# Kernel tuning notes

Measured on AMD Instinct MI355X. Metric: run time of the kernel, lower is better.

Reference implementation:

```python
import jax, jax.numpy as jnp
import numpy as np

B, N, S, C1, C2 = 8, 8192, 2048, 128, 256
IN_CH = C1 + C2
MLP = [256, 128]
EPS_INTERP = 1e-8
EPS_BN = 1e-5


def setup_inputs() -> dict:
    key = jax.random.key(0)
    ks = jax.random.split(key, 8)
    inp = {
        "xyz1": jax.random.normal(ks[0], (B, 3, N), dtype=jnp.float32),
        "xyz2": jax.random.normal(ks[1], (B, 3, S), dtype=jnp.float32),
        "points1": jax.random.normal(ks[2], (B, C1, N), dtype=jnp.float32),
        "points2": jax.random.normal(ks[3], (B, C2, S), dtype=jnp.float32),
        # Conv1d(k=1) weights as [out, in] matrices, plus BN gamma/beta
        "W1": jax.random.normal(ks[4], (MLP[0], IN_CH), dtype=jnp.float32) * 0.02,
        "b1": jnp.zeros((MLP[0],), dtype=jnp.float32),
        "g1": jnp.ones((MLP[0],), dtype=jnp.float32),
        "be1": jnp.zeros((MLP[0],), dtype=jnp.float32),
        "W2": jax.random.normal(ks[5], (MLP[1], MLP[0]), dtype=jnp.float32) * 0.02,
        "b2": jnp.zeros((MLP[1],), dtype=jnp.float32),
        "g2": jnp.ones((MLP[1],), dtype=jnp.float32),
        "be2": jnp.zeros((MLP[1],), dtype=jnp.float32),
    }
    return inp


def _conv_bn_relu(x, W, b, g, be):
    # x: [B, N, Cin]; 1x1 Conv1d == per-point matmul; BN over (batch, length) per channel (training-mode stats)
    y = jnp.einsum('bnc,oc->bno', x, W) + b
    m = jnp.mean(y, axis=(0, 1))
    v = jnp.var(y, axis=(0, 1))
    return jax.nn.relu((y - m) * jax.lax.rsqrt(v + EPS_BN) * g + be)


def reference(xyz1, xyz2, points1, points2, W1, b1, g1, be1, W2, b2, g2, be2):
    x1 = xyz1.transpose(0, 2, 1)   # [B, N, 3]
    x2 = xyz2.transpose(0, 2, 1)   # [B, S, 3]
    p2 = points2.transpose(0, 2, 1)  # [B, S, C2]
    p1 = points1.transpose(0, 2, 1)  # [B, N, C1]

    # squared pairwise distances [B, N, S]
    d = (jnp.sum(x1 * x1, axis=-1, keepdims=True)
         - 2.0 * jnp.einsum('bnd,bsd->bns', x1, x2)
         + jnp.sum(x2 * x2, axis=-1)[:, None, :])

    # 3 nearest neighbors (smallest distances)
    neg_d, idx = jax.lax.top_k(-d, 3)          # idx: [B, N, 3]
    d3 = -neg_d                                 # [B, N, 3]
    recip = 1.0 / (d3 + EPS_INTERP)
    w = recip / jnp.sum(recip, axis=-1, keepdims=True)  # [B, N, 3]

    gathered = jax.vmap(lambda p, i: p[i])(p2, idx)     # [B, N, 3, C2]
    interp = jnp.sum(gathered * w[..., None], axis=2)   # [B, N, C2]

    x = jnp.concatenate([p1, interp], axis=-1)          # [B, N, C1+C2]
    x = _conv_bn_relu(x, W1, b1, g1, be1)
    x = _conv_bn_relu(x, W2, b2, g2, be2)
    return x.transpose(0, 2, 1)                         # [B, mlp[-1], N]
```

## Files before the change

kernel.cpp:

```cpp
#include <hip/hip_runtime.h>
#include <stdint.h>

#define B_ 8
#define N_ 8192
#define S_ 2048
#define C1_ 128
#define C2_ 256
#define IN_ 384
#define H1_ 256
#define H2_ 128
#define M_ (B_*N_)

typedef short bf16x8 __attribute__((ext_vector_type(8)));
typedef float f32x4 __attribute__((ext_vector_type(4)));

__device__ __forceinline__ float bf2f(unsigned short s){
  union { unsigned int u; float f; } x; x.u = ((unsigned int)s) << 16; return x.f;
}
__device__ __forceinline__ unsigned short f2bf(float f){
  union { float f; unsigned int u; } x; x.f = f;
  unsigned int u = x.u;
  unsigned int r = (u + 0x7FFFu + ((u >> 16) & 1u)) >> 16;
  return (unsigned short)r;
}

__device__ __forceinline__ size_t fragaddr(int m, int k, int K){
  return ((size_t)((m >> 4) * (K >> 5) + (k >> 5)) << 9)
       + (size_t)((((k >> 3) & 3) << 7) + ((m & 15) << 3) + (k & 7));
}

__device__ __forceinline__ void gload_lds16(const unsigned short* g, unsigned short* l){
  __builtin_amdgcn_global_load_lds(
      (const __attribute__((address_space(1))) unsigned int*)g,
      (__attribute__((address_space(3))) unsigned int*)l, 16, 0, 0);
}

__global__ __launch_bounds__(256) void prep_fused_kernel(const float* W1, const float* W2,
                                                         const float* p2, const float* p1,
                                                         const float* xyz2, float4* ptsg,
                                                         unsigned short* w1b, unsigned short* w2b,
                                                         float* stats, unsigned short* p2t,
                                                         unsigned short* x){
  __shared__ float tile[32][33];
  int bx = blockIdx.x;
  if (bx < 384){
    int i = bx * 256 + threadIdx.x;
    if (i < 256*384){
      int row = i / 384, col = i - row*384;
      w1b[fragaddr(row, col, 384)] = f2bf(W1[i]);
    }
    if (i < 128*256){
      int row = i >> 8, col = i & 255;
      w2b[fragaddr(row, col, 256)] = f2bf(W2[i]);
    }
    if (i < 1536) stats[i] = 0.f;
    return;
  }
  if (bx < 448){
    int i = (bx - 384) * 256 + threadIdx.x;
    int b = i >> 11, s = i & 2047;
    const float* src = xyz2 + (size_t)b * 3 * S_;
    float px = src[s], py = src[S_ + s], pz = src[2*S_ + s];
    ptsg[i] = make_float4(-2.f*px, -2.f*py, -2.f*pz, px*px + py*py + pz*pz);
    return;
  }
  int tx = threadIdx.x & 31, ty = threadIdx.x >> 5;
  if (bx < 4544){
    int id = bx - 448;
    int b = id >> 9, rem = id & 511;
    int l0 = (rem & 63) * 32, r0 = (rem >> 6) * 32;
    const float* src = p2 + (size_t)b * C2_ * S_;
    #pragma unroll
    for (int rr = ty; rr < 32; rr += 8)
      tile[rr][tx] = src[(size_t)(r0 + rr) * S_ + l0 + tx];
    __syncthreads();
    unsigned short* dst = p2t + (size_t)b * S_ * C2_;
    #pragma unroll
    for (int rr = ty; rr < 32; rr += 8)
      dst[(size_t)(l0 + rr) * C2_ + r0 + tx] = f2bf(tile[tx][rr]);
    return;
  }
  {
    int id = bx - 4544;
    int b = id >> 10, rem = id & 1023;
    int l0 = (rem & 255) * 32, r0 = (rem >> 8) * 32;
    const float* src = p1 + (size_t)b * C1_ * N_;
    #pragma unroll
    for (int rr = ty; rr < 32; rr += 8)
      tile[rr][tx] = src[(size_t)(r0 + rr) * N_ + l0 + tx];
    __syncthreads();
    #pragma unroll
    for (int rr = ty; rr < 32; rr += 8){
      int g = b * N_ + l0 + rr;
      size_t a = ((size_t)((g >> 4)*12 + (r0 >> 5)) << 9)
               + (size_t)((((tx >> 3) & 3) << 7) + ((g & 15) << 3) + (tx & 7));
      x[a] = f2bf(tile[tx][rr]);
    }
  }
}

#define PIECES_ 8
#define SPP_ (S_ / PIECES_)

__device__ __forceinline__ void insert_k(float& k0, float& k1, float& k2, float x){
  k2 = __builtin_amdgcn_fmed3f(k1, k2, x);
  k1 = __builtin_amdgcn_fmed3f(k0, k1, x);
  k0 = fminf(k0, x);
}

__device__ __forceinline__ void insert3(float& d0, float& d1, float& d2,
                                        int& i0, int& i1, int& i2,
                                        float x, int s){
  bool b0 = x < d0, b1 = x < d1, b2 = x < d2;
  i2 = b1 ? i1 : (b2 ? s : i2);
  i1 = b0 ? i0 : (b1 ? s : i1);
  i0 = b0 ? s : i0;
  d2 = __builtin_amdgcn_fmed3f(d1, d2, x);
  d1 = __builtin_amdgcn_fmed3f(d0, d1, x);
  d0 = fminf(d0, x);
}

__global__ __launch_bounds__(256, 8) void knn_kernel(const float* __restrict__ xyz1,
                                                     const float4* __restrict__ ptsg,
                                                     float* __restrict__ partd,
                                                     int* __restrict__ parti){
  __shared__ float4 pts[SPP_];
  int b = blockIdx.y, piece = blockIdx.z;
  int n = blockIdx.x * 256 + threadIdx.x;
  int base = piece * SPP_;
  const float4* __restrict__ cp = ptsg + (size_t)b * S_ + base;
  pts[threadIdx.x] = cp[threadIdx.x];

  const float* __restrict__ x1 = xyz1 + (size_t)b * 3 * N_;
  float ax = x1[n], ay = x1[N_ + n], az = x1[2*N_ + n];
  float x1sq = ax*ax + ay*ay + az*az;

  const float KINIT = __uint_as_float(0x7F000000u);
  float k[2][3];
  k[0][0]=k[0][1]=k[0][2]=KINIT;
  k[1][0]=k[1][1]=k[1][2]=KINIT;

  for (int s = 0; s < SPP_; s += 8){
    #pragma unroll
    for (int u = 0; u < 8; u++){
      float4 c = cp[s + u];
      float dd = fmaf(ax, c.x, fmaf(ay, c.y, fmaf(az, c.z, c.w + x1sq)));
      float key = __uint_as_float((__float_as_uint(dd) & 0xFFFFFF00u) | (unsigned)(s + u));
      int L = u & 1;
      insert_k(k[L][0], k[L][1], k[L][2], key);
    }
  }
  float e0 = k[0][0], e1 = k[0][1], e2 = k[0][2];
  insert_k(e0, e1, e2, k[1][0]);
  insert_k(e0, e1, e2, k[1][1]);
  insert_k(e0, e1, e2, k[1][2]);

  __syncthreads();
  float ed[3]; int ei[3];
  float ev[3] = {e0, e1, e2};
  #pragma unroll
  for (int j = 0; j < 3; j++){
    int li = (int)(__float_as_uint(ev[j]) & 0xFFu);
    float4 c = pts[li];
    float dd = fmaf(ax, c.x, fmaf(ay, c.y, fmaf(az, c.z, c.w + x1sq)));
    ed[j] = fmaxf(dd, 0.f);
    ei[j] = base + li;
  }

  size_t g = (size_t)b * N_ + n;
  partd[(piece*3 + 0)*(size_t)M_ + g] = ed[0];
  partd[(piece*3 + 1)*(size_t)M_ + g] = ed[1];
  partd[(piece*3 + 2)*(size_t)M_ + g] = ed[2];
  parti[(piece*3 + 0)*(size_t)M_ + g] = ei[0];
  parti[(piece*3 + 1)*(size_t)M_ + g] = ei[1];
  parti[(piece*3 + 2)*(size_t)M_ + g] = ei[2];
}

__global__ __launch_bounds__(256) void interp_kernel(const float* partd, const int* parti,
                                                     const unsigned short* p2t, unsigned short* x){
  __shared__ int   sidx[16][3];
  __shared__ float swgt[16][3];
  int t = threadIdx.x;
  int base = blockIdx.x * 16;
  if (t < 16){
    size_t g = (size_t)base + t;
    float d0 = partd[0*(size_t)M_ + g], d1 = partd[1*(size_t)M_ + g], d2 = partd[2*(size_t)M_ + g];
    int   i0 = parti[0*(size_t)M_ + g], i1 = parti[1*(size_t)M_ + g], i2 = parti[2*(size_t)M_ + g];
    #pragma unroll
    for (int p = 1; p < PIECES_; p++)
      #pragma unroll
      for (int j = 0; j < 3; j++)
        insert3(d0, d1, d2, i0, i1, i2,
                partd[(p*3 + j)*(size_t)M_ + g], parti[(p*3 + j)*(size_t)M_ + g]);
    float r0 = 1.f/(d0 + 1e-8f), r1 = 1.f/(d1 + 1e-8f), r2 = 1.f/(d2 + 1e-8f);
    float rs = 1.f/(r0 + r1 + r2);
    sidx[t][0] = i0; sidx[t][1] = i1; sidx[t][2] = i2;
    swgt[t][0] = r0*rs; swgt[t][1] = r1*rs; swgt[t][2] = r2*rs;
  }
  __syncthreads();
  size_t suboff = (size_t)((((t >> 3) & 3) << 7) + (t & 7));
  for (int k = 0; k < 16; k++){
    int g = base + k;
    int b = g >> 13;
    const unsigned short* p = p2t + (size_t)b * S_ * C2_;
    float v = swgt[k][0]*bf2f(p[(size_t)sidx[k][0]*C2_ + t])
            + swgt[k][1]*bf2f(p[(size_t)sidx[k][1]*C2_ + t])
            + swgt[k][2]*bf2f(p[(size_t)sidx[k][2]*C2_ + t]);
    size_t a = ((size_t)((g >> 4)*12 + 4 + (t >> 5)) << 9) + suboff + (size_t)((g & 15) << 3);
    x[a] = f2bf(v);
  }
}

__device__ __forceinline__ bf16x8 bn_relu_frag(bf16x8 v, const float* a, const float* c, int kb){
  union { bf16x8 h; unsigned short s[8]; } u; u.h = v;
  union { float4 v4; float f[4]; } a0, a1, c0, c1;
  a0.v4 = *(const float4*)(a + kb);  a1.v4 = *(const float4*)(a + kb + 4);
  c0.v4 = *(const float4*)(c + kb);  c1.v4 = *(const float4*)(c + kb + 4);
  #pragma unroll
  for (int j = 0; j < 4; j++){
    float f0 = fmaf(a0.f[j], bf2f(u.s[j]),     c0.f[j]);
    float f1 = fmaf(a1.f[j], bf2f(u.s[j + 4]), c1.f[j]);
    u.s[j]     = f2bf(fmaxf(f0, 0.f));
    u.s[j + 4] = f2bf(fmaxf(f1, 0.f));
  }
  return u.h;
}

template<int K, bool HAS_AFF, bool OUT_FRAG>
__global__ __launch_bounds__(256) void gemm_lds_kernel(
    const unsigned short* __restrict__ A, const unsigned short* __restrict__ Wf,
    unsigned short* __restrict__ Cout, int Ntot,
    float* sumv, float* sqv, const float* aff_a, const float* aff_c)
{
  constexpr int KT = K / 32;
  __shared__ unsigned short smA[128*64];
  __shared__ unsigned short smB[128*64];
  __shared__ float ldsStat[256];

  const int t = threadIdx.x;
  const int lane = t & 63, wave = t >> 6;
  const int ln = lane & 15, lq = lane >> 4;
  const int wm = wave >> 1, wn = wave & 1;
  const int mtb = blockIdx.x * 8;
  const int ntb = blockIdx.y * 8;
  const int mtw = mtb + wm * 4;
  const int n0  = blockIdx.y * 128 + wn * 64;

  ldsStat[t] = 0.f;

  const int c0 = 2*wave, c1 = 2*wave + 1;

  const f32x4 fzero = {0.f, 0.f, 0.f, 0.f};
  f32x4 acc[4][4];
  #pragma unroll
  for (int i = 0; i < 4; i++)
    #pragma unroll
    for (int j = 0; j < 4; j++) acc[i][j] = fzero;

  for (int kk = 0; kk < KT; kk += 2){
    #pragma unroll
    for (int q = 0; q < 2; q++){
      gload_lds16(A  + (((size_t)((mtb + c0)*KT + kk + q)) << 9) + lane*8,
                  &smA[((c0*2 + q) << 9) + lane*8]);
      gload_lds16(A  + (((size_t)((mtb + c1)*KT + kk + q)) << 9) + lane*8,
                  &smA[((c1*2 + q) << 9) + lane*8]);
      gload_lds16(Wf + (((size_t)((ntb + c0)*KT + kk + q)) << 9) + lane*8,
                  &smB[((c0*2 + q) << 9) + lane*8]);
      gload_lds16(Wf + (((size_t)((ntb + c1)*KT + kk + q)) << 9) + lane*8,
                  &smB[((c1*2 + q) << 9) + lane*8]);
    }
    __syncthreads();
    #pragma unroll
    for (int q = 0; q < 2; q++){
      bf16x8 af[4], bf[4];
      #pragma unroll
      for (int i = 0; i < 4; i++)
        af[i] = *(const bf16x8*)(&smA[(((wm*4 + i)*2 + q) << 9) + lane*8]);
      #pragma unroll
      for (int j = 0; j < 4; j++)
        bf[j] = *(const bf16x8*)(&smB[(((wn*4 + j)*2 + q) << 9) + lane*8]);
      if (HAS_AFF){
        const int kb = (kk + q)*32 + lq*8;
        #pragma unroll
        for (int i = 0; i < 4; i++) af[i] = bn_relu_frag(af[i], aff_a, aff_c, kb);
      }
      #pragma unroll
      for (int i = 0; i < 4; i++)
        #pragma unroll
        for (int j = 0; j < 4; j++)
          acc[i][j] = __builtin_amdgcn_mfma_f32_16x16x32_bf16(af[i], bf[j], acc[i][j], 0, 0, 0);
    }
    __syncthreads();
  }

  #pragma unroll
  for (int j = 0; j < 4; j++){
    int ncol = n0 + j*16 + ln;
    float s = 0.f, q = 0.f;
    #pragma unroll
    for (int i = 0; i < 4; i++){
      #pragma unroll
      for (int r = 0; r < 4; r++){
        float v = acc[i][j][r];
        if (OUT_FRAG){
          size_t a = ((size_t)((mtw + i)*8 + (ncol >> 5)) << 9)
                   + (size_t)((((ncol >> 3) & 3) << 7) + ((lq*4 + r) << 3) + (ncol & 7));
          Cout[a] = f2bf(v);
        } else {
          Cout[((size_t)((mtw + i)*16 + lq*4 + r)) * Ntot + ncol] = f2bf(v);
        }
        s += v; q += v*v;
      }
    }
    s += __shfl_xor(s, 16); s += __shfl_xor(s, 32);
    q += __shfl_xor(q, 16); q += __shfl_xor(q, 32);
    if (lq == 0){
      int colLocal = wn*64 + j*16 + ln;
      atomicAdd(&ldsStat[colLocal], s);
      atomicAdd(&ldsStat[128 + colLocal], q);
    }
  }
  __syncthreads();
  {
    float v = ldsStat[t];
    int col = blockIdx.y*128 + (t & 127);
    atomicAdd((t < 128 ? &sumv[col] : &sqv[col]), v);
  }
}

__global__ void finalize_kernel(const float* sum, const float* sq, const float* g, const float* be,
                                float* a_out, float* c_out, int C){
  int c = threadIdx.x;
  if (c < C){
    float mean = sum[c] * (1.f / M_);
    float var  = sq[c]  * (1.f / M_) - mean*mean;
    float a = g[c] * rsqrtf(var + 1e-5f);
    a_out[c] = a;
    c_out[c] = fmaf(-mean, a, be[c]);
  }
}

__global__ __launch_bounds__(256) void out_kernel(const unsigned short* y2, const float* a2,
                                                  const float* c2, float* out){
  __shared__ float lds[64][65];
  int t  = threadIdx.x;
  int b  = blockIdx.z;
  int n0 = blockIdx.y * 64;
  int c0 = blockIdx.x * 64;
  int cc = t & 63, tr = t >> 6;
  float a = a2[c0 + cc], cadd = c2[c0 + cc];
  #pragma unroll
  for (int ph = 0; ph < 16; ph++){
    int nr = tr + ph*4;
    unsigned short v = y2[((size_t)(b*N_ + n0 + nr)) * H2_ + c0 + cc];
    lds[nr][cc] = fmaxf(fmaf(a, bf2f(v), cadd), 0.f);
  }
  __syncthreads();
  #pragma unroll
  for (int ph = 0; ph < 16; ph++){
    int cr = tr + ph*4;
    out[((size_t)(b*H2_ + c0 + cr)) * N_ + n0 + cc] = lds[cc][cr];
  }
}

extern "C" void kernel_launch(void* const* d_in, const int* in_sizes, int n_in,
                              void* d_out, int out_size, void* d_ws, size_t ws_size,
                              hipStream_t stream){
  const float* xyz1 = (const float*)d_in[0];
  const float* xyz2 = (const float*)d_in[1];
  const float* p1   = (const float*)d_in[2];
  const float* p2   = (const float*)d_in[3];
  const float* W1   = (const float*)d_in[4];
  const float* g1   = (const float*)d_in[6];
  const float* be1  = (const float*)d_in[7];
  const float* W2   = (const float*)d_in[8];
  const float* g2   = (const float*)d_in[10];
  const float* be2  = (const float*)d_in[11];
  float* out = (float*)d_out;

  char* ws = (char*)d_ws;
  unsigned short* x    = (unsigned short*)(ws + 0);
  unsigned short* p2t  = (unsigned short*)(ws + 50331648);
  unsigned short* y1   = (unsigned short*)(ws + 58720256);
  unsigned short* y2   = (unsigned short*)(ws + 92274688);
  unsigned short* w1b  = (unsigned short*)(ws + 109051904);
  unsigned short* w2b  = (unsigned short*)(ws + 109248512);
  float*          stats= (float*)(ws + 110886912);
  float* sum1 = stats;        float* sq1 = stats + 256;
  float* sum2 = stats + 512;  float* sq2 = stats + 640;
  float* a1   = stats + 768;  float* c1  = stats + 1024;
  float* a2   = stats + 1280; float* c2  = stats + 1408;
  float* partd = (float*)y1;
  int*   parti = (int*)(y1 + 6291456);
  float4* ptsg = (float4*)y2;

  prep_fused_kernel<<<12736, 256, 0, stream>>>(W1, W2, p2, p1, xyz2, ptsg, w1b, w2b, stats, p2t, x);
  knn_kernel<<<dim3(32, 8, PIECES_), 256, 0, stream>>>(xyz1, ptsg, partd, parti);
  interp_kernel<<<4096, 256, 0, stream>>>(partd, parti, p2t, x);
  gemm_lds_kernel<384, false, true><<<dim3(512, 2), 256, 0, stream>>>(
      x, w1b, y1, 256, sum1, sq1, nullptr, nullptr);
  finalize_kernel<<<1, 256, 0, stream>>>(sum1, sq1, g1, be1, a1, c1, 256);
  gemm_lds_kernel<256, true, false><<<dim3(512, 1), 256, 0, stream>>>(
      y1, w2b, y2, 128, sum2, sq2, a1, c1);
  finalize_kernel<<<1, 256, 0, stream>>>(sum2, sq2, g2, be2, a2, c2, 128);
  out_kernel<<<dim3(2, 128, 8), 256, 0, stream>>>(y2, a2, c2, out);
}
```

Baseline: 265.7 us.

## Double-buffer LDS tiles in GEMM to overlap global loads with MFMA

Splits the A and B shared-memory tiles into two buffers and issues the global-to-LDS loads for the next K step before computing on the current one. This is meant to hide load latency behind the MFMA work and cut one barrier per iteration. In exchange LDS use doubles to about 64KB per block, which may lower occupancy, and the loop is now fully unrolled.

```diff
diff --git a/kernel.cpp b/kernel.cpp
--- a/kernel.cpp
+++ b/kernel.cpp
@@ -233,8 +233,9 @@
     float* sumv, float* sqv, const float* aff_a, const float* aff_c)
 {
   constexpr int KT = K / 32;
-  __shared__ unsigned short smA[128*64];
-  __shared__ unsigned short smB[128*64];
+  constexpr int NI = KT / 2;
+  __shared__ unsigned short smA[2][128*64];
+  __shared__ unsigned short smB[2][128*64];
   __shared__ float ldsStat[256];
 
   const int t = threadIdx.x;
@@ -250,6 +251,20 @@
 
   const int c0 = 2*wave, c1 = 2*wave + 1;
 
+  auto stage = [&](int buf, int kk){
+    #pragma unroll
+    for (int q = 0; q < 2; q++){
+      gload_lds16(A  + (((size_t)((mtb + c0)*KT + kk + q)) << 9) + lane*8,
+                  &smA[buf][((c0*2 + q) << 9) + lane*8]);
+      gload_lds16(A  + (((size_t)((mtb + c1)*KT + kk + q)) << 9) + lane*8,
+                  &smA[buf][((c1*2 + q) << 9) + lane*8]);
+      gload_lds16(Wf + (((size_t)((ntb + c0)*KT + kk + q)) << 9) + lane*8,
+                  &smB[buf][((c0*2 + q) << 9) + lane*8]);
+      gload_lds16(Wf + (((size_t)((ntb + c1)*KT + kk + q)) << 9) + lane*8,
+                  &smB[buf][((c1*2 + q) << 9) + lane*8]);
+    }
+  };
+
   const f32x4 fzero = {0.f, 0.f, 0.f, 0.f};
   f32x4 acc[4][4];
   #pragma unroll
@@ -257,28 +272,23 @@
     #pragma unroll
     for (int j = 0; j < 4; j++) acc[i][j] = fzero;
 
-  for (int kk = 0; kk < KT; kk += 2){
+  stage(0, 0);
+  __syncthreads();
+
+  #pragma unroll
+  for (int it = 0; it < NI; ++it){
+    const int cur = it & 1;
+    if (it + 1 < NI) stage(cur ^ 1, (it + 1)*2);
+    const int kk = it*2;
     #pragma unroll
     for (int q = 0; q < 2; q++){
-      gload_lds16(A  + (((size_t)((mtb + c0)*KT + kk + q)) << 9) + lane*8,
-                  &smA[((c0*2 + q) << 9) + lane*8]);
-      gload_lds16(A  + (((size_t)((mtb + c1)*KT + kk + q)) << 9) + lane*8,
-                  &smA[((c1*2 + q) << 9) + lane*8]);
-      gload_lds16(Wf + (((size_t)((ntb + c0)*KT + kk + q)) << 9) + lane*8,
-                  &smB[((c0*2 + q) << 9) + lane*8]);
-      gload_lds16(Wf + (((size_t)((ntb + c1)*KT + kk + q)) << 9) + lane*8,
-                  &smB[((c1*2 + q) << 9) + lane*8]);
-    }
-    __syncthreads();
-    #pragma unroll
-    for (int q = 0; q < 2; q++){
-      bf16x8 af[4], bf[4];
+      bf16x8 af[4], bfr[4];
       #pragma unroll
       for (int i = 0; i < 4; i++)
-        af[i] = *(const bf16x8*)(&smA[(((wm*4 + i)*2 + q) << 9) + lane*8]);
+        af[i] = *(const bf16x8*)(&smA[cur][(((wm*4 + i)*2 + q) << 9) + lane*8]);
       #pragma unroll
       for (int j = 0; j < 4; j++)
-        bf[j] = *(const bf16x8*)(&smB[(((wn*4 + j)*2 + q) << 9) + lane*8]);
+        bfr[j] = *(const bf16x8*)(&smB[cur][(((wn*4 + j)*2 + q) << 9) + lane*8]);
       if (HAS_AFF){
         const int kb = (kk + q)*32 + lq*8;
         #pragma unroll
@@ -288,7 +298,7 @@
       for (int i = 0; i < 4; i++)
         #pragma unroll
         for (int j = 0; j < 4; j++)
-          acc[i][j] = __builtin_amdgcn_mfma_f32_16x16x32_bf16(af[i], bf[j], acc[i][j], 0, 0, 0);
+          acc[i][j] = __builtin_amdgcn_mfma_f32_16x16x32_bf16(af[i], bfr[j], acc[i][j], 0, 0, 0);
     }
     __syncthreads();
   }
```

Measured after the change: 274.5 us. 1.03x slower.
